# Performance work log

Measured on AMD Instinct MI355X. Metric: run time of the kernel, lower is better.

The kernel has to match this reference:

```python
import jax, jax.numpy as jnp
import numpy as np

B, T, C = 4, 2048, 1024
N_HEADS = 16
HEAD_DIM = C // N_HEADS


def rotary_embedding(seq_len, dim, dtype=jnp.float32):
    pos = jnp.arange(seq_len, dtype=dtype)[:, None]
    i = jnp.arange(0, dim, 2, dtype=dtype)[None, :]
    theta = pos / jnp.power(10000.0, i / dim)
    return jnp.cos(theta), jnp.sin(theta)


def apply_rotary(x, cos, sin):
    # x: [B, T, H, D]; cos/sin: [T, D//2]
    d = x.shape[-1]
    x1, x2 = x[..., : d // 2], x[..., d // 2 :]
    rotated = jnp.concatenate([-x2, x1], axis=-1)
    cos = jnp.concatenate([cos, cos], axis=-1)[None, :, None, :]
    sin = jnp.concatenate([sin, sin], axis=-1)[None, :, None, :]
    return x * cos + rotated * sin


def setup_inputs() -> dict:
    key = jax.random.key(0)
    k1, k2, k3 = jax.random.split(key, 3)
    x = jax.random.normal(k1, (B, T, C), dtype=jnp.float32)
    # lecun_normal-ish init scale
    w_qkv = jax.random.normal(k2, (C, 3 * C), dtype=jnp.float32) / np.sqrt(C)
    w_out = jax.random.normal(k3, (C, C), dtype=jnp.float32) / np.sqrt(C)
    return {"x": x, "w_qkv": w_qkv, "w_out": w_out}


def reference(x, w_qkv, w_out):
    b, t, c = x.shape
    qkv = jnp.einsum("btc,cd->btd", x, w_qkv)
    q, k, v = jnp.split(qkv, 3, axis=-1)
    q = q.reshape(b, t, N_HEADS, HEAD_DIM)
    k = k.reshape(b, t, N_HEADS, HEAD_DIM)
    v = v.reshape(b, t, N_HEADS, HEAD_DIM)
    cos, sin = rotary_embedding(t, HEAD_DIM, dtype=x.dtype)
    q = apply_rotary(q, cos, sin)
    k = apply_rotary(k, cos, sin)
    scale = jnp.sqrt(jnp.asarray(HEAD_DIM, dtype=x.dtype))
    # scores: [B, H, T, T]
    attn = jnp.einsum("bqhd,bkhd->bhqk", q, k) / scale
    mask = jnp.tril(jnp.ones((t, t), dtype=jnp.bool_))
    attn = jnp.where(mask[None, None, :, :], attn, jnp.asarray(-1e9, dtype=x.dtype))
    attn = jax.nn.softmax(attn, axis=-1)
    out = jnp.einsum("bhqk,bkhd->bqhd", attn, v).reshape(b, t, c)
    return jnp.einsum("btc,cd->btd", out, w_out)
```

## Files before the change

### kernel.cpp

```cpp
#include <hip/hip_runtime.h>
#include <stdint.h>

#define DEVI __device__ __forceinline__

typedef unsigned short ushort_t;
typedef __bf16 bf16x8 __attribute__((ext_vector_type(8)));
typedef float f32x4 __attribute__((ext_vector_type(4)));
typedef unsigned short ushort8 __attribute__((ext_vector_type(8)));
typedef short s16x4 __attribute__((ext_vector_type(4)));

#define BB 4
#define TT 2048
#define CC 1024
#define NH 16
#define HD 64
#define MM (BB*TT)

DEVI ushort_t f2bf(float f) {
    union { float f; unsigned u; } v; v.f = f;
    return (ushort_t)((v.u + 0x7FFFu + ((v.u >> 16) & 1u)) >> 16);
}

typedef const __attribute__((address_space(1))) unsigned int guint_t;
typedef __attribute__((address_space(3))) unsigned int luint_t;

DEVI void gl2lds16(const void* g, void* lds) {
    __builtin_amdgcn_global_load_lds((guint_t*)(uintptr_t)g,
                                     (luint_t*)(unsigned int)(uintptr_t)lds,
                                     16, 0, 0);
}

__global__ void cvt_f32_bf16(const float* __restrict__ in,
                             ushort_t* __restrict__ out) {
    int i = blockIdx.x * 256 + threadIdx.x;
    const float4* p = (const float4*)in + (size_t)i * 2;
    float4 a = p[0], b = p[1];
    ushort8 r;
    r[0] = f2bf(a.x); r[1] = f2bf(a.y); r[2] = f2bf(a.z); r[3] = f2bf(a.w);
    r[4] = f2bf(b.x); r[5] = f2bf(b.y); r[6] = f2bf(b.z); r[7] = f2bf(b.w);
    *(ushort8*)(out + (size_t)i * 8) = r;
}

__global__ void transpose_f2b(const float* __restrict__ in,
                              ushort_t* __restrict__ out, int R, int Cc) {
    __shared__ ushort_t tile[32][33];
    int bx = blockIdx.x * 32;
    int by = blockIdx.y * 32;
    int tx = threadIdx.x & 31, ty = threadIdx.x >> 5;
    #pragma unroll
    for (int i = 0; i < 4; i++) {
        int r = ty * 4 + i;
        tile[r][tx] = f2bf(in[(size_t)(by + r) * Cc + bx + tx]);
    }
    __syncthreads();
    #pragma unroll
    for (int i = 0; i < 4; i++) {
        int r = ty * 4 + i;
        out[(size_t)(bx + r) * R + by + tx] = tile[tx][r];
    }
}

__global__ void rope_table(float2* __restrict__ tab) {
    int i = blockIdx.x * 256 + threadIdx.x;
    int t = i >> 5, j = i & 31;
    float inv = exp2f((float)j * -0.41524101186092029f);
    float theta = (float)t * inv;
    float s, c;
    sincosf(theta, &s, &c);
    tab[i] = make_float2(c, s);
}

__global__ void vtrans(const ushort_t* __restrict__ Vb,
                       ushort_t* __restrict__ VbT) {
    __shared__ ushort_t tile[64 * 72];
    const int bh = blockIdx.y;
    const int t0 = blockIdx.x * 64;
    const int tid = threadIdx.x;
    const int r = tid >> 2, c = (tid & 3) * 16;
    const size_t base = (size_t)bh * (TT * HD);
    const ushort_t* g = Vb + base + (size_t)(t0 + r) * HD + c;
    *(ushort8*)&tile[r * 72 + c]     = *(const ushort8*)g;
    *(ushort8*)&tile[r * 72 + c + 8] = *(const ushort8*)(g + 8);
    __syncthreads();
    ushort8 a, b;
    #pragma unroll
    for (int j = 0; j < 8; j++) a[j] = tile[(c + j) * 72 + r];
    #pragma unroll
    for (int j = 0; j < 8; j++) b[j] = tile[(c + 8 + j) * 72 + r];
    ushort_t* o = VbT + base + (size_t)r * TT + t0 + c;
    *(ushort8*)o = a;
    *(ushort8*)(o + 8) = b;
}

template <int MODE>
__global__ __launch_bounds__(256, 2) void gemm_bt(
    const ushort_t* __restrict__ A, const ushort_t* __restrict__ Bt,
    float* __restrict__ CoutF,
    ushort_t* __restrict__ Qb, ushort_t* __restrict__ Kb, ushort_t* __restrict__ Vb,
    const float2* __restrict__ rope, int M, int N, int Kd) {
    __shared__ __attribute__((aligned(16))) ushort_t As[128 * 32];
    __shared__ __attribute__((aligned(16))) ushort_t Bs[128 * 32];

    const int tid = threadIdx.x;
    const int w = tid >> 6, l = tid & 63;
    const int lane15 = l & 15, quad = l >> 4;
    const int wm = (w >> 1) * 64, wn = (w & 1) * 64;
    const int bm = blockIdx.y, bn = blockIdx.x;

    f32x4 acc[4][4];
    #pragma unroll
    for (int i = 0; i < 4; i++)
        #pragma unroll
        for (int j = 0; j < 4; j++)
            acc[i][j] = f32x4{0.f, 0.f, 0.f, 0.f};

    const int c0 = w * 2, c1 = w * 2 + 1;
    const int lr = l >> 2, lc = (l & 3) * 8;
    const int rowA0 = bm * 128 + c0 * 16 + lr;
    const int rowA1 = bm * 128 + c1 * 16 + lr;
    const ushort_t *gA0, *gA1;
    if (MODE == 2) {
        gA0 = A + ((size_t)(rowA0 >> 11) * 32768 + (rowA0 & (TT - 1))) * HD + lc;
        gA1 = A + ((size_t)(rowA1 >> 11) * 32768 + (rowA1 & (TT - 1))) * HD + lc;
    } else {
        gA0 = A + (size_t)rowA0 * Kd + lc;
        gA1 = A + (size_t)rowA1 * Kd + lc;
    }
    const ushort_t* gB0 = Bt + (size_t)(bn * 128 + c0 * 16 + lr) * Kd + lc;
    const ushort_t* gB1 = Bt + (size_t)(bn * 128 + c1 * 16 + lr) * Kd + lc;

    for (int k0 = 0; k0 < Kd; k0 += 32) {
        size_t offA = (MODE == 2) ? ((size_t)(k0 >> 6) * 131072 + (size_t)(k0 & 63))
                                  : (size_t)k0;
        __syncthreads();
        gl2lds16(gA0 + offA, &As[c0 * 512]);
        gl2lds16(gA1 + offA, &As[c1 * 512]);
        gl2lds16(gB0 + k0,  &Bs[c0 * 512]);
        gl2lds16(gB1 + k0,  &Bs[c1 * 512]);
        __syncthreads();

        bf16x8 af[4], bf[4];
        #pragma unroll
        for (int t = 0; t < 4; t++) {
            af[t] = *(const bf16x8*)&As[(wm + t * 16 + lane15) * 32 + quad * 8];
            bf[t] = *(const bf16x8*)&Bs[(wn + t * 16 + lane15) * 32 + quad * 8];
        }
        #pragma unroll
        for (int tm = 0; tm < 4; tm++)
            #pragma unroll
            for (int tn = 0; tn < 4; tn++)
                acc[tm][tn] = __builtin_amdgcn_mfma_f32_16x16x32_bf16(
                    af[tm], bf[tn], acc[tm][tn], 0, 0, 0);
    }

    if (MODE == 2) {
        #pragma unroll
        for (int tm = 0; tm < 4; tm++) {
            int row0 = bm * 128 + wm + tm * 16 + quad * 4;
            #pragma unroll
            for (int r = 0; r < 4; r++) {
                size_t rb = (size_t)(row0 + r) * N + bn * 128 + wn;
                #pragma unroll
                for (int tn = 0; tn < 4; tn++)
                    CoutF[rb + tn * 16 + lane15] = acc[tm][tn][r];
            }
        }
    } else {
        const float SCQ = 0.125f * 1.4426950408889634f;
        const int colbase = bn * 128 + wn;
        const int seg = colbase >> 10;
        const int h = (colbase & 1023) >> 6;
        #pragma unroll
        for (int tm = 0; tm < 4; tm++) {
            int row0 = bm * 128 + wm + tm * 16 + quad * 4;
            #pragma unroll
            for (int r = 0; r < 4; r++) {
                int row = row0 + r;
                int b = row >> 11, t = row & (TT - 1);
                size_t ob = ((size_t)(b * NH + h) * TT + t) * HD;
                if (seg == 2) {
                    #pragma unroll
                    for (int tn = 0; tn < 4; tn++)
                        Vb[ob + tn * 16 + lane15] = f2bf(acc[tm][tn][r]);
                } else {
                    ushort_t* dst = (seg == 0) ? Qb : Kb;
                    #pragma unroll
                    for (int tn = 0; tn < 2; tn++) {
                        int j = tn * 16 + lane15;
                        float2 cs = rope[t * 32 + j];
                        float x1 = acc[tm][tn][r];
                        float x2 = acc[tm][tn + 2][r];
                        float y1 = x1 * cs.x - x2 * cs.y;
                        float y2 = x2 * cs.x + x1 * cs.y;
                        if (seg == 0) { y1 *= SCQ; y2 *= SCQ; }
                        dst[ob + j]      = f2bf(y1);
                        dst[ob + 32 + j] = f2bf(y2);
                    }
                }
            }
        }
    }
}

__global__ __launch_bounds__(512, 4) void attn_kernel(
    ushort_t* __restrict__ Qb, const ushort_t* __restrict__ Kb,
    const ushort_t* __restrict__ VbT) {
    __shared__ __attribute__((aligned(16))) ushort_t Ks[64 * 72];
    __shared__ __attribute__((aligned(16))) ushort_t Vs[64 * 72];

    const int tid = threadIdx.x;
    const int w = tid >> 6, l = tid & 63;
    const int lane15 = l & 15, quad = l >> 4;
    const int bh = blockIdx.y;
    const size_t base = (size_t)bh * (TT * HD);

    const int sr = tid >> 3;
    const int sd = (tid & 7) * 8;
    const ushort_t* kgb = Kb  + base + (size_t)sr * HD + sd;
    const ushort_t* vgb = VbT + base + (size_t)sr * TT + sd;

    #pragma unroll
    for (int seg = 0; seg < 2; seg++) {
        const int qt = (seg == 0) ? (int)blockIdx.x : (15 - (int)blockIdx.x);
        const int q0 = qt * 128;
        const int rbase = q0 + w * 16;
        const int ktmax = 2 * qt + 1;

        bf16x8 qf0, qf1;
        {
            const ushort_t* qp = Qb + base + (size_t)(rbase + lane15) * HD + quad * 8;
            qf0 = *(const bf16x8*)qp;
            qf1 = *(const bf16x8*)(qp + 32);
        }

        f32x4 o[4];
        #pragma unroll
        for (int nt = 0; nt < 4; nt++) o[nt] = f32x4{0.f, 0.f, 0.f, 0.f};
        float mrow = -INFINITY, lrow = 0.f;

        ushort8 kr = *(const ushort8*)kgb;
        ushort8 vr = *(const ushort8*)vgb;

        for (int kt = 0; kt <= ktmax; kt++) {
            __syncthreads();
            *(ushort8*)&Ks[sr * 72 + sd] = kr;
            *(ushort8*)&Vs[sr * 72 + sd] = vr;
            __syncthreads();
            if (kt < ktmax) {
                kr = *(const ushort8*)(kgb + (size_t)(kt + 1) * 64 * HD);
                vr = *(const ushort8*)(vgb + (size_t)(kt + 1) * 64);
            }

            f32x4 s[4];
            #pragma unroll
            for (int c = 0; c < 4; c++) {
                bf16x8 k0 = *(const bf16x8*)&Ks[(c * 16 + lane15) * 72 + quad * 8];
                bf16x8 k1 = *(const bf16x8*)&Ks[(c * 16 + lane15) * 72 + 32 + quad * 8];
                f32x4 z = f32x4{0.f, 0.f, 0.f, 0.f};
                z = __builtin_amdgcn_mfma_f32_16x16x32_bf16(k0, qf0, z, 0, 0, 0);
                s[c] = __builtin_amdgcn_mfma_f32_16x16x32_bf16(k1, qf1, z, 0, 0, 0);
            }

            const int qrow = rbase + lane15;
            if (kt * 64 + 63 > rbase) {
                #pragma unroll
                for (int c = 0; c < 4; c++)
                    #pragma unroll
                    for (int r = 0; r < 4; r++)
                        if (kt * 64 + c * 16 + quad * 4 + r > qrow) s[c][r] = -1e9f;
            }

            float mt = s[0][0];
            #pragma unroll
            for (int c = 0; c < 4; c++)
                #pragma unroll
                for (int r = 0; r < 4; r++) mt = fmaxf(mt, s[c][r]);
            mt = fmaxf(mt, __shfl_xor(mt, 16, 64));
            mt = fmaxf(mt, __shfl_xor(mt, 32, 64));

            float mn = fmaxf(mrow, mt);
            float alpha = __builtin_amdgcn_exp2f(mrow - mn);
            mrow = mn;

            #pragma unroll
            for (int c = 0; c < 4; c++)
                #pragma unroll
                for (int r = 0; r < 4; r++)
                    s[c][r] = __builtin_amdgcn_exp2f(s[c][r] - mn);

            float rs = 0.f;
            #pragma unroll
            for (int c = 0; c < 4; c++)
                rs += (s[c][0] + s[c][1]) + (s[c][2] + s[c][3]);
            rs += __shfl_xor(rs, 16, 64);
            rs += __shfl_xor(rs, 32, 64);
            lrow = lrow * alpha + rs;

            #pragma unroll
            for (int r = 0; r < 4; r++) {
                float aO = __shfl(alpha, quad * 4 + r, 64);
                #pragma unroll
                for (int nt = 0; nt < 4; nt++) o[nt][r] *= aO;
            }

            #pragma unroll
            for (int c = 0; c < 4; c++) {
                s16x4 pf;
                #pragma unroll
                for (int r = 0; r < 4; r++) pf[r] = (short)f2bf(s[c][r]);
                #pragma unroll
                for (int nt = 0; nt < 4; nt++) {
                    s16x4 vf = *(const s16x4*)&Vs[(nt * 16 + lane15) * 72 +
                                                  c * 16 + quad * 4];
                    o[nt] = __builtin_amdgcn_mfma_f32_16x16x16bf16_1k(
                        pf, vf, o[nt], 0, 0, 0);
                }
            }
        }

        float linv = 1.0f / lrow;
        #pragma unroll
        for (int r = 0; r < 4; r++) {
            float lO = __shfl(linv, quad * 4 + r, 64);
            size_t rb = base + (size_t)(rbase + quad * 4 + r) * HD;
            #pragma unroll
            for (int nt = 0; nt < 4; nt++)
                Qb[rb + nt * 16 + lane15] = f2bf(o[nt][r] * lO);
        }
    }
}

extern "C" void kernel_launch(void* const* d_in, const int* in_sizes, int n_in,
                              void* d_out, int out_size, void* d_ws, size_t ws_size,
                              hipStream_t stream) {
    const float* x    = (const float*)d_in[0];
    const float* wqkv = (const float*)d_in[1];
    const float* wout = (const float*)d_in[2];
    float* out = (float*)d_out;

    char* ws = (char*)d_ws;
    ushort_t* WqkvT = (ushort_t*)(ws);
    ushort_t* WoutT = (ushort_t*)(ws + 6291456);
    float2*   rope  = (float2*)  (ws + 8388608);
    ushort_t* Xb    = (ushort_t*)(ws + 8912896);
    ushort_t* Qb    = (ushort_t*)(ws + 8912896 + 16777216);
    ushort_t* Kb    = (ushort_t*)(ws + 8912896 + 2 * 16777216);
    ushort_t* Vb    = (ushort_t*)(ws + 8912896 + 3 * 16777216);
    ushort_t* VbT   = Xb;

    cvt_f32_bf16<<<dim3(MM * CC / (256 * 8)), 256, 0, stream>>>(x, Xb);
    transpose_f2b<<<dim3(3 * CC / 32, CC / 32), 256, 0, stream>>>(wqkv, WqkvT, CC, 3 * CC);
    transpose_f2b<<<dim3(CC / 32, CC / 32), 256, 0, stream>>>(wout, WoutT, CC, CC);
    rope_table<<<dim3(256), 256, 0, stream>>>(rope);

    gemm_bt<1><<<dim3(3 * CC / 128, MM / 128), 256, 0, stream>>>(
        Xb, WqkvT, nullptr, Qb, Kb, Vb, rope, MM, 3 * CC, CC);

    vtrans<<<dim3(TT / 64, BB * NH), 256, 0, stream>>>(Vb, VbT);

    attn_kernel<<<dim3(8, BB * NH), 512, 0, stream>>>(Qb, Kb, VbT);

    gemm_bt<2><<<dim3(CC / 128, MM / 128), 256, 0, stream>>>(
        Qb, WoutT, out, nullptr, nullptr, nullptr, nullptr, MM, CC, CC);
}
```

Baseline: 281.1 us.

## Rewrite GEMM with double-buffered LDS, XOR swizzle, larger tiles and grid remap

Reworks the shared bf16 GEMM used for the QKV and output projections. It uses 512-thread blocks with 128x256 tiles and a k-step of 64. The kernel double-buffers LDS with explicit vmcnt waits so global-to-LDS loads overlap MFMA work, and it XOR-swizzles the LDS layout to avoid bank conflicts. It also remaps block IDs across the grid for better L2 locality and raises MFMA wave priority. The trade-offs are more LDS per block, fewer blocks (occupancy and tail effects), and hardcoded vmcnt literals and K=1024 assumptions.

```diff
diff --git a/kernel.cpp b/kernel.cpp
--- a/kernel.cpp
+++ b/kernel.cpp
@@ -28,6 +28,13 @@
     __builtin_amdgcn_global_load_lds((guint_t*)(uintptr_t)g,
                                      (luint_t*)(unsigned int)(uintptr_t)lds,
                                      16, 0, 0);
+}
+
+template <int N> DEVI void waitvm() {
+    static_assert(N == 0 || N == 6 || N == 8, "unsupported vmcnt literal");
+    if constexpr (N == 0)      asm volatile("s_waitcnt vmcnt(0)" ::: "memory");
+    else if constexpr (N == 6) asm volatile("s_waitcnt vmcnt(6)" ::: "memory");
+    else if constexpr (N == 8) asm volatile("s_waitcnt vmcnt(8)" ::: "memory");
 }
 
 __global__ void cvt_f32_bf16(const float* __restrict__ in,
@@ -92,104 +99,135 @@
     *(ushort8*)(o + 8) = b;
 }
 
-template <int MODE>
-__global__ __launch_bounds__(256, 2) void gemm_bt(
+template <int MODE, int BM>
+__global__ __launch_bounds__(512, 2) void gemm_bt(
     const ushort_t* __restrict__ A, const ushort_t* __restrict__ Bt,
     float* __restrict__ CoutF,
     ushort_t* __restrict__ Qb, ushort_t* __restrict__ Kb, ushort_t* __restrict__ Vb,
     const float2* __restrict__ rope, int M, int N, int Kd) {
-    __shared__ __attribute__((aligned(16))) ushort_t As[128 * 32];
-    __shared__ __attribute__((aligned(16))) ushort_t Bs[128 * 32];
+    constexpr int MR = BM / 32;
+    constexpr int AL = BM / 64;
+    constexpr int L  = AL + 4;
+    constexpr int NK = CC / 64;
+    (void)M;
+
+    __shared__ __attribute__((aligned(16))) ushort_t As[2][BM * 64];
+    __shared__ __attribute__((aligned(16))) ushort_t Bs[2][256 * 64];
 
     const int tid = threadIdx.x;
     const int w = tid >> 6, l = tid & 63;
     const int lane15 = l & 15, quad = l >> 4;
-    const int wm = (w >> 1) * 64, wn = (w & 1) * 64;
-    const int bm = blockIdx.y, bn = blockIdx.x;
-
-    f32x4 acc[4][4];
-    #pragma unroll
-    for (int i = 0; i < 4; i++)
-        #pragma unroll
-        for (int j = 0; j < 4; j++)
-            acc[i][j] = f32x4{0.f, 0.f, 0.f, 0.f};
-
-    const int c0 = w * 2, c1 = w * 2 + 1;
-    const int lr = l >> 2, lc = (l & 3) * 8;
-    const int rowA0 = bm * 128 + c0 * 16 + lr;
-    const int rowA1 = bm * 128 + c1 * 16 + lr;
-    const ushort_t *gA0, *gA1;
-    if (MODE == 2) {
-        gA0 = A + ((size_t)(rowA0 >> 11) * 32768 + (rowA0 & (TT - 1))) * HD + lc;
-        gA1 = A + ((size_t)(rowA1 >> 11) * 32768 + (rowA1 & (TT - 1))) * HD + lc;
-    } else {
-        gA0 = A + (size_t)rowA0 * Kd + lc;
-        gA1 = A + (size_t)rowA1 * Kd + lc;
+    const int wm = (w >> 2) * (BM / 2);
+    const int wn = (w & 3) * 64;
+
+    const int nbn = gridDim.x;
+    const int nwg = nbn * gridDim.y;
+    const int lid = blockIdx.y * nbn + blockIdx.x;
+    const int sid = (lid & 7) * (nwg >> 3) + (lid >> 3);
+    const int bn = sid % nbn, bm = sid / nbn;
+
+    const int sr8 = l >> 3;
+    const int sc  = l & 7;
+
+    auto STAGE = [&](int buf, int k0) {
+        #pragma unroll
+        for (int i = 0; i < AL; ++i) {
+            int r = w * (BM / 8) + i * 8 + sr8;
+            int gr = bm * BM + r;
+            size_t e;
+            if constexpr (MODE == 2)
+                e = ((size_t)(gr >> 11)) * 2097152 + ((size_t)(k0 >> 6)) * 131072
+                    + (size_t)(gr & (TT - 1)) * 64;
+            else
+                e = (size_t)gr * Kd + k0;
+            const char* g = (const char*)(A + e) + ((sc ^ sr8) * 16);
+            gl2lds16(g, (char*)&As[buf][0] + (w * (BM / 8) + i * 8) * 128);
+        }
+        #pragma unroll
+        for (int i = 0; i < 4; ++i) {
+            int r = w * 32 + i * 8 + sr8;
+            int gr = bn * 256 + r;
+            const char* g = (const char*)(Bt + (size_t)gr * Kd + k0)
+                            + ((sc ^ sr8) * 16);
+            gl2lds16(g, (char*)&Bs[buf][0] + (w * 32 + i * 8) * 128);
+        }
+    };
+
+    f32x4 acc[MR][4];
+    #pragma unroll
+    for (int m = 0; m < MR; ++m)
+        #pragma unroll
+        for (int n = 0; n < 4; ++n)
+            acc[m][n] = f32x4{0.f, 0.f, 0.f, 0.f};
+
+    STAGE(0, 0);
+    STAGE(1, 64);
+    waitvm<L>();
+    __builtin_amdgcn_s_barrier();
+    asm volatile("" ::: "memory");
+
+    const int swz = (lane15 & 7) << 4;
+
+    for (int k = 0; k < NK; ++k) {
+        const char* Asb = (const char*)&As[k & 1][0];
+        const char* Bsb = (const char*)&Bs[k & 1][0];
+        #pragma unroll
+        for (int kk = 0; kk < 2; ++kk) {
+            const int cb = (kk * 64 + quad * 16) ^ swz;
+            bf16x8 bfr[4];
+            #pragma unroll
+            for (int n = 0; n < 4; ++n)
+                bfr[n] = *(const bf16x8*)(Bsb + (wn + n * 16 + lane15) * 128 + cb);
+            bf16x8 af[MR];
+            #pragma unroll
+            for (int m = 0; m < MR; ++m)
+                af[m] = *(const bf16x8*)(Asb + (wm + m * 16 + lane15) * 128 + cb);
+            __builtin_amdgcn_s_setprio(1);
+            #pragma unroll
+            for (int m = 0; m < MR; ++m)
+                #pragma unroll
+                for (int n = 0; n < 4; ++n)
+                    acc[m][n] = __builtin_amdgcn_mfma_f32_16x16x32_bf16(
+                        af[m], bfr[n], acc[m][n], 0, 0, 0);
+            __builtin_amdgcn_s_setprio(0);
+        }
+        if (k == NK - 1) break;
+
+        __builtin_amdgcn_sched_barrier(0);
+        asm volatile("s_waitcnt lgkmcnt(0)" ::: "memory");
+        __builtin_amdgcn_s_barrier();
+        asm volatile("" ::: "memory");
+        if (k + 2 < NK) { STAGE(k & 1, (k + 2) * 64); waitvm<L>(); }
+        else            waitvm<0>();
+        __builtin_amdgcn_s_barrier();
+        asm volatile("" ::: "memory");
     }
-    const ushort_t* gB0 = Bt + (size_t)(bn * 128 + c0 * 16 + lr) * Kd + lc;
-    const ushort_t* gB1 = Bt + (size_t)(bn * 128 + c1 * 16 + lr) * Kd + lc;
-
-    for (int k0 = 0; k0 < Kd; k0 += 32) {
-        size_t offA = (MODE == 2) ? ((size_t)(k0 >> 6) * 131072 + (size_t)(k0 & 63))
-                                  : (size_t)k0;
-        __syncthreads();
-        gl2lds16(gA0 + offA, &As[c0 * 512]);
-        gl2lds16(gA1 + offA, &As[c1 * 512]);
-        gl2lds16(gB0 + k0,  &Bs[c0 * 512]);
-        gl2lds16(gB1 + k0,  &Bs[c1 * 512]);
-        __syncthreads();
-
-        bf16x8 af[4], bf[4];
-        #pragma unroll
-        for (int t = 0; t < 4; t++) {
-            af[t] = *(const bf16x8*)&As[(wm + t * 16 + lane15) * 32 + quad * 8];
-            bf[t] = *(const bf16x8*)&Bs[(wn + t * 16 + lane15) * 32 + quad * 8];
-        }
-        #pragma unroll
-        for (int tm = 0; tm < 4; tm++)
-            #pragma unroll
-            for (int tn = 0; tn < 4; tn++)
-                acc[tm][tn] = __builtin_amdgcn_mfma_f32_16x16x32_bf16(
-                    af[tm], bf[tn], acc[tm][tn], 0, 0, 0);
-    }
-
-    if (MODE == 2) {
-        #pragma unroll
-        for (int tm = 0; tm < 4; tm++) {
-            int row0 = bm * 128 + wm + tm * 16 + quad * 4;
-            #pragma unroll
-            for (int r = 0; r < 4; r++) {
-                size_t rb = (size_t)(row0 + r) * N + bn * 128 + wn;
-                #pragma unroll
-                for (int tn = 0; tn < 4; tn++)
-                    CoutF[rb + tn * 16 + lane15] = acc[tm][tn][r];
-            }
-        }
-    } else {
+
+    if constexpr (MODE == 1) {
         const float SCQ = 0.125f * 1.4426950408889634f;
-        const int colbase = bn * 128 + wn;
+        const int colbase = bn * 256 + wn;
         const int seg = colbase >> 10;
         const int h = (colbase & 1023) >> 6;
         #pragma unroll
-        for (int tm = 0; tm < 4; tm++) {
-            int row0 = bm * 128 + wm + tm * 16 + quad * 4;
-            #pragma unroll
-            for (int r = 0; r < 4; r++) {
+        for (int m = 0; m < MR; ++m) {
+            int row0 = bm * BM + wm + m * 16 + quad * 4;
+            #pragma unroll
+            for (int r = 0; r < 4; ++r) {
                 int row = row0 + r;
                 int b = row >> 11, t = row & (TT - 1);
                 size_t ob = ((size_t)(b * NH + h) * TT + t) * HD;
                 if (seg == 2) {
                     #pragma unroll
-                    for (int tn = 0; tn < 4; tn++)
-                        Vb[ob + tn * 16 + lane15] = f2bf(acc[tm][tn][r]);
+                    for (int n = 0; n < 4; ++n)
+                        Vb[ob + n * 16 + lane15] = f2bf(acc[m][n][r]);
                 } else {
                     ushort_t* dst = (seg == 0) ? Qb : Kb;
                     #pragma unroll
-                    for (int tn = 0; tn < 2; tn++) {
-                        int j = tn * 16 + lane15;
+                    for (int n = 0; n < 2; ++n) {
+                        int j = n * 16 + lane15;
                         float2 cs = rope[t * 32 + j];
-                        float x1 = acc[tm][tn][r];
-                        float x2 = acc[tm][tn + 2][r];
+                        float x1 = acc[m][n][r];
+                        float x2 = acc[m][n + 2][r];
                         float y1 = x1 * cs.x - x2 * cs.y;
                         float y2 = x2 * cs.x + x1 * cs.y;
                         if (seg == 0) { y1 *= SCQ; y2 *= SCQ; }
@@ -197,6 +235,18 @@
                         dst[ob + 32 + j] = f2bf(y2);
                     }
                 }
+            }
+        }
+    } else {
+        #pragma unroll
+        for (int m = 0; m < MR; ++m) {
+            #pragma unroll
+            for (int r = 0; r < 4; ++r) {
+                size_t rb = (size_t)(bm * BM + wm + m * 16 + quad * 4 + r) * N
+                            + bn * 256 + wn;
+                #pragma unroll
+                for (int n = 0; n < 4; ++n)
+                    CoutF[rb + n * 16 + lane15] = acc[m][n][r];
             }
         }
     }
@@ -353,13 +403,13 @@
     transpose_f2b<<<dim3(CC / 32, CC / 32), 256, 0, stream>>>(wout, WoutT, CC, CC);
     rope_table<<<dim3(256), 256, 0, stream>>>(rope);
 
-    gemm_bt<1><<<dim3(3 * CC / 128, MM / 128), 256, 0, stream>>>(
+    gemm_bt<1, 128><<<dim3(3 * CC / 256, MM / 128), 512, 0, stream>>>(
         Xb, WqkvT, nullptr, Qb, Kb, Vb, rope, MM, 3 * CC, CC);
 
     vtrans<<<dim3(TT / 64, BB * NH), 256, 0, stream>>>(Vb, VbT);
 
     attn_kernel<<<dim3(8, BB * NH), 512, 0, stream>>>(Qb, Kb, VbT);
 
-    gemm_bt<2><<<dim3(CC / 128, MM / 128), 256, 0, stream>>>(
+    gemm_bt<2, 128><<<dim3(CC / 256, MM / 128), 512, 0, stream>>>(
         Qb, WoutT, out, nullptr, nullptr, nullptr, nullptr, MM, CC, CC);
 }
```

Measured after the change: 274.5 us. 2.4% less time.
